# Optimization experiments

Hardware: AMD Instinct MI355X
Metric: run time of the kernel (lower is better)

The kernel has to match this reference:

```python
import jax, jax.numpy as jnp
import numpy as np

TEMP = 0.07  # temperature used as logits / 0.07 in the original


def setup_inputs() -> dict:
    key = jax.random.key(0)
    k1, k2, k3 = jax.random.split(key, 3)
    B, N, T, L, D = 8, 128, 8, 6, 256
    meta = jax.random.normal(k1, (B, N, T, L, D), dtype=jnp.float32)
    thing = jax.random.randint(k2, (B, N, T), 0, 2, dtype=jnp.int32)
    label = jax.random.randint(k3, (B, N, T), 0, 40, dtype=jnp.int32)
    return {"meta_weight_for_con": meta, "thing_gt_idx": thing, "label_tmp": label}


def _con_loss(meta, thing, label):
    # meta: [B,N,T,L,D]; thing,label: [B,N,T]
    B, N, T, L, D = meta.shape
    P = N * T
    valid = thing.reshape(B, P).astype(bool)            # [B,P] boolean gt mask
    lab = label.reshape(B, P)                           # [B,P]
    # meta_weight_b[mask] -> [K,L,D]; permute(1,0,2) -> per-layer [K,D].
    # We keep all P positions and mask instead of compacting (jit-friendly).
    w = meta.reshape(B, P, L, D).transpose(0, 2, 1, 3)  # [B,L,P,D]
    w = w / jnp.maximum(jnp.linalg.norm(w, axis=-1, keepdims=True), 1e-12)  # F.normalize
    z = jnp.einsum('blpd,blqd->blpq', w, w) / TEMP      # similarity / temp [B,L,P,P]

    same = lab[:, :, None] == lab[:, None, :]           # [B,P,P]
    vpair = valid[:, :, None] & valid[:, None, :]
    eye = jnp.eye(P, dtype=bool)
    pos_mask = same & (~eye) & vpair                    # positives: same label, not self
    neg_mask = (~same) & vpair                          # negatives: different label

    K = valid.sum(axis=1)                               # [B] ins_num_ per batch
    pos_count = pos_mask.sum(axis=-1)                   # [B,P]
    neg_count = neg_mask.sum(axis=-1)                   # [B,P]

    # --- random positive sample per (batch, layer, row), mirroring np.random.choice ---
    u = jax.random.uniform(jax.random.key(42), (B, L, P))
    r = jnp.floor(u * pos_count[:, None, :].astype(u.dtype)).astype(jnp.int32)
    r = jnp.minimum(r, jnp.maximum(pos_count - 1, 0)[:, None, :])
    ranks = jnp.cumsum(pos_mask, axis=-1) - 1           # rank of each positive in index order
    sel = pos_mask[:, None, :, :] & (ranks[:, None, :, :] == r[..., None])  # [B,L,P,P]
    zp = jnp.sum(jnp.where(sel, z, 0.0), axis=-1)       # chosen positive logit [B,L,P]
    diag = jnp.diagonal(z, axis1=-2, axis2=-1)          # self-sim fallback when no positives
    zp = jnp.where((pos_count > 0)[:, None, :], zp, diag)

    # --- last negative (original pads by repeating the last negative to K-1) ---
    iota = jnp.arange(P)
    idx_last = jnp.max(jnp.where(neg_mask, iota[None, None, :], -1), axis=-1)  # [B,P]
    idx = jnp.broadcast_to(jnp.maximum(idx_last, 0)[:, None, :, None], (B, L, P, 1))
    zl = jnp.take_along_axis(z, idx, axis=-1)[..., 0]   # [B,L,P]

    # --- stable CE with label 0: loss = lse(logits) - zp ---
    max_n = jnp.max(jnp.where(neg_mask[:, None], z, -jnp.inf), axis=-1)  # [B,L,P]
    m = jnp.maximum(zp, max_n)
    m = jnp.where(jnp.isfinite(m), m, zp)
    sum_neg = jnp.sum(jnp.where(neg_mask[:, None], jnp.exp(z - m[..., None]), 0.0), axis=-1)
    pad = jnp.maximum((K[:, None] - 1 - neg_count), 0).astype(z.dtype)   # [B,P]
    pad_term = pad[:, None, :] * jnp.where((neg_count > 0)[:, None, :], jnp.exp(zl - m), 0.0)
    loss_row = m + jnp.log(jnp.exp(zp - m) + sum_neg + pad_term) - zp    # [B,L,P]

    row_w = valid.astype(z.dtype)
    mean_per = jnp.sum(loss_row * row_w[:, None, :], axis=-1) / jnp.maximum(K, 1)[:, None].astype(z.dtype)  # [B,L]

    gate = jnp.sum((thing.sum(axis=2) > 0), axis=1) >= 2  # skip batches with <2 gt rows
    return jnp.sum(jnp.where(gate[:, None], mean_per, 0.0))


def reference(meta_weight_for_con, thing_gt_idx, label_tmp):
    return _con_loss(meta_weight_for_con, thing_gt_idx, label_tmp)
```

## Files before the change

kernel.cpp:

```cpp
#include <hip/hip_runtime.h>
#include <stdint.h>

namespace {

constexpr int Bb = 8, Ll = 6, Dd = 256, Pp = 1024;
constexpr float SCALE_Y = 14.285714285714286f * 1.4426950408889634f;
constexpr float M0y = 21.0f;
constexpr float LN2f = 0.6931471805599453f;

typedef __attribute__((ext_vector_type(4))) float floatx4;

__device__ const int PAIRS[36] = {
  0x00,0x01,0x02,0x03,0x04,0x05,0x06,0x07,
  0x11,0x12,0x13,0x14,0x15,0x16,0x17,
  0x22,0x23,0x24,0x25,0x26,0x27,
  0x33,0x34,0x35,0x36,0x37,
  0x44,0x45,0x46,0x47,
  0x55,0x56,0x57,
  0x66,0x67,
  0x77
};

__device__ __forceinline__ void async16(const void* g, void* l) {
  __builtin_amdgcn_global_load_lds(
      (const __attribute__((address_space(1))) void*)g,
      (__attribute__((address_space(3))) void*)l, 16, 0, 0);
}

__device__ __forceinline__ uint32_t rotl32(uint32_t x, int n) {
  return (x << n) | (x >> (32 - n));
}
__device__ __forceinline__ void tf_round(uint32_t& x0, uint32_t& x1, int r) {
  x0 += x1; x1 = rotl32(x1, r); x1 ^= x0;
}
__device__ void threefry2x32(uint32_t x0, uint32_t x1, uint32_t& o0, uint32_t& o1) {
  const uint32_t k0 = 0u, k1 = 42u;
  const uint32_t k2 = k0 ^ k1 ^ 0x1BD11BDAu;
  x0 += k0; x1 += k1;
  tf_round(x0,x1,13); tf_round(x0,x1,15); tf_round(x0,x1,26); tf_round(x0,x1,6);
  x0 += k1; x1 += k2 + 1u;
  tf_round(x0,x1,17); tf_round(x0,x1,29); tf_round(x0,x1,16); tf_round(x0,x1,24);
  x0 += k2; x1 += k0 + 2u;
  tf_round(x0,x1,13); tf_round(x0,x1,15); tf_round(x0,x1,26); tf_round(x0,x1,6);
  x0 += k0; x1 += k1 + 3u;
  tf_round(x0,x1,17); tf_round(x0,x1,29); tf_round(x0,x1,16); tf_round(x0,x1,24);
  x0 += k1; x1 += k2 + 4u;
  tf_round(x0,x1,13); tf_round(x0,x1,15); tf_round(x0,x1,26); tf_round(x0,x1,6);
  x0 += k2; x1 += k0 + 5u;
  o0 = x0; o1 = x1;
}
__device__ float jax_u01(uint32_t idx) {
  const uint32_t HALF = (uint32_t)(Bb * Ll * Pp / 2);
  uint32_t o0, o1, bits;
  if (idx < HALF) { threefry2x32(idx, idx + HALF, o0, o1); bits = o0; }
  else            { threefry2x32(idx - HALF, idx, o0, o1); bits = o1; }
  return __uint_as_float((bits >> 9) | 0x3f800000u) - 1.0f;
}

__device__ __forceinline__ uint32_t fp8e4m3_rne(float x) {
  uint32_t u = __float_as_uint(x);
  const uint32_t s = (u >> 24) & 0x80u;
  u &= 0x7FFFFFFFu;
  uint32_t code;
  if (u < 0x3C800000u) {
    code = (uint32_t)__float2int_rn(__uint_as_float(u) * 512.0f);
  } else {
    const uint32_t r = (u + 0x7FFFFu + ((u >> 20) & 1u)) >> 20;
    code = r - (120u << 3);
  }
  return s | code;
}
__device__ __forceinline__ float fp8e4m3_tof(uint32_t c) {
  const uint32_t e = (c >> 3) & 15u, m = c & 7u;
  float mag;
  if (e) mag = __uint_as_float(((e + 120u) << 23) | (m << 20));
  else   mag = (float)m * 0.001953125f;
  return (c & 0x80u) ? -mag : mag;
}

constexpr int NB_NORM = Bb * Pp * Ll / 4;
constexpr int NB_ROW  = Bb * Pp / 4;

__global__ void prep_k(const float* __restrict__ meta, const int* __restrict__ thing,
                       const int* __restrict__ label, uint8_t* __restrict__ wn,
                       int* __restrict__ qpos, int* __restrict__ negc,
                       int* __restrict__ qidx, int* __restrict__ Kv,
                       int* __restrict__ gatev, float* __restrict__ rowsum_g,
                       int* __restrict__ cnt, float* __restrict__ out) {
  __shared__ int sK[256], sG[256];
  const int bid = blockIdx.x, t = threadIdx.x;

  if (bid < NB_NORM) {
    const int wid = (bid * 256 + t) >> 6;
    const int lane = t & 63;
    const float4 v = *(const float4*)(meta + (size_t)wid * Dd + lane * 4);
    float ss = v.x * v.x + v.y * v.y + v.z * v.z + v.w * v.w;
    #pragma unroll
    for (int m = 32; m; m >>= 1) ss += __shfl_xor(ss, m, 64);
    const float inv = 1.0f / fmaxf(sqrtf(ss), 1e-12f);
    const int bp = wid / Ll, l = wid - bp * Ll;
    const int b = bp >> 10, p = bp & (Pp - 1);
    uint8_t* dst = wn + ((size_t)(b * Ll + l) * Pp + p) * Dd + lane * 4;
    const uint32_t packed = fp8e4m3_rne(v.x * inv)
                          | (fp8e4m3_rne(v.y * inv) << 8)
                          | (fp8e4m3_rne(v.z * inv) << 16)
                          | (fp8e4m3_rne(v.w * inv) << 24);
    *(uint32_t*)dst = packed;
    return;
  }
  if (bid < NB_NORM + NB_ROW) {
    const int wid = (bid - NB_NORM) * 4 + (t >> 6);
    const int lane = t & 63;
    const int b = wid >> 10, p = wid & (Pp - 1);
    const int* lab = label + b * Pp;
    const int* th  = thing + b * Pp;
    const int myLab = lab[p];
    const bool myValid = (th[p] != 0);

    uint32_t posbits = 0;
    int cntc[16];
    int pc = 0, nc = 0, last = -1;
    #pragma unroll
    for (int c = 0; c < 16; ++c) {
      const int q = c * 64 + lane;
      const int lq = lab[q];
      const bool vq = (th[q] != 0);
      const bool same = (lq == myLab);
      const bool pos = myValid && vq && same && (q != p);
      const bool neg = myValid && vq && !same;
      uint64_t bp2 = __ballot(pos);
      uint64_t bn = __ballot(neg);
      if (pos) posbits |= (1u << c);
      cntc[c] = __popcll(bp2);
      pc += cntc[c];
      nc += __popcll(bn);
      if (bn) last = c * 64 + 63 - __clzll(bn);
    }
    int qsel[Ll];
    #pragma unroll
    for (int l = 0; l < Ll; ++l) qsel[l] = p;
    if (pc > 0) {
      for (int l = 0; l < Ll; ++l) {
        const float u = jax_u01((uint32_t)((b * Ll + l) * Pp + p));
        int r = (int)floorf(u * (float)pc);
        r = min(r, pc - 1);
        int base = 0;
        for (int c = 0; c < 16; ++c) {
          if (r < base + cntc[c]) {
            const bool mine = (posbits >> c) & 1u;
            uint64_t bm = __ballot(mine);
            uint64_t ltmask = (lane == 0) ? 0ull : (~0ull >> (64 - lane));
            int myrank = __popcll(bm & ltmask);
            bool hit = mine && (base + myrank == r);
            uint64_t hb = __ballot(hit);
            qsel[l] = c * 64 + (int)__builtin_ctzll(hb);
            break;
          }
          base += cntc[c];
        }
      }
    }
    if (lane == 0) {
      negc[wid] = nc;
      qidx[wid] = (last < 0) ? 0 : last;
      #pragma unroll
      for (int l = 0; l < Ll; ++l) qpos[(b * Ll + l) * Pp + p] = qsel[l];
    }
    return;
  }
  if (bid < NB_NORM + NB_ROW + Bb) {
    const int b = bid - (NB_NORM + NB_ROW);
    int k = 0;
    for (int p = t; p < Pp; p += 256) k += (thing[b * Pp + p] != 0);
    int g = 0;
    if (t < 128) {
      int any = 0;
      for (int tt = 0; tt < 8; ++tt) any |= (thing[(b * 128 + t) * 8 + tt] != 0);
      g = any;
    }
    sK[t] = k; sG[t] = g;
    __syncthreads();
    for (int s = 128; s; s >>= 1) {
      if (t < s) { sK[t] += sK[t + s]; sG[t] += sG[t + s]; }
      __syncthreads();
    }
    if (t == 0) { Kv[b] = sK[0]; gatev[b] = (sG[0] >= 2) ? 1 : 0; }
    return;
  }
  if (bid < NB_NORM + NB_ROW + Bb + 48) {
    const int idx = (bid - (NB_NORM + NB_ROW + Bb)) * 256 + t;
    *(float4*)(rowsum_g + idx * 4) = (float4){0.f, 0.f, 0.f, 0.f};
    return;
  }
  if (t == 0) out[0] = 0.f;
  if (t < 48) cnt[t] = 0;
}

__global__ void zpzl_k(const uint8_t* __restrict__ wn,
                       const int* __restrict__ qpos, const int* __restrict__ qidx,
                       float* __restrict__ zp_g, float* __restrict__ zl_g) {
  const int wid = blockIdx.x * 4 + (threadIdx.x >> 6);
  const int lane = threadIdx.x & 63;
  const int bl = wid >> 10, p = wid & (Pp - 1);
  const int b = bl / Ll;
  const int qp = qpos[bl * Pp + p];
  const int qi = qidx[b * Pp + p];
  const uint8_t* W = wn + (size_t)bl * Pp * Dd;
  const uint32_t a4 = *(const uint32_t*)(W + (size_t)p  * Dd + lane * 4);
  const uint32_t b4 = *(const uint32_t*)(W + (size_t)qp * Dd + lane * 4);
  const uint32_t c4 = *(const uint32_t*)(W + (size_t)qi * Dd + lane * 4);
  float sp = 0.f, sl = 0.f;
  #pragma unroll
  for (int i = 0; i < 4; ++i) {
    const float a = fp8e4m3_tof((a4 >> (8 * i)) & 0xFF);
    sp += a * fp8e4m3_tof((b4 >> (8 * i)) & 0xFF);
    sl += a * fp8e4m3_tof((c4 >> (8 * i)) & 0xFF);
  }
  #pragma unroll
  for (int m = 32; m; m >>= 1) {
    sp += __shfl_xor(sp, m, 64);
    sl += __shfl_xor(sl, m, 64);
  }
  if (lane == 0) {
    zp_g[bl * Pp + p] = sp * SCALE_Y;
    zl_g[bl * Pp + p] = sl * SCALE_Y;
  }
}

__global__ __launch_bounds__(256)
void gemm_loss_k(const uint8_t* __restrict__ wn,
                 const int* __restrict__ thing, const int* __restrict__ label,
                 float* __restrict__ rowsum_g, const float* __restrict__ zp_g,
                 const float* __restrict__ zl_g, const int* __restrict__ negc,
                 const int* __restrict__ Kv, const int* __restrict__ gatev,
                 int* __restrict__ cnt, float* __restrict__ out) {
  __shared__ __align__(16) uint8_t As[128 * 256];
  __shared__ __align__(16) uint8_t Bs[128 * 256];
  __shared__ int labp_s[128], valp_s[128], labq_s[128], valq_s[128];
  __shared__ float rowsum_lds[128], colsum_lds[128];
  __shared__ int last_s;

  const int t = threadIdx.x;
  const int bid = blockIdx.x;
  const int xcd = bid & 7;
  const int chunk = bid >> 3;
  const int bl = xcd + 8 * (chunk % 6);
  const int b = bl / Ll;
  const int pair = PAIRS[chunk / 6];
  const int pt = pair >> 4, qt = pair & 15;
  const bool diag = (pt == qt);
  const int p0 = pt * 128, q0 = qt * 128;

  if (t < 128) {
    labp_s[t] = label[b * Pp + p0 + t];
    valp_s[t] = thing[b * Pp + p0 + t];
    labq_s[t] = label[b * Pp + q0 + t];
    valq_s[t] = thing[b * Pp + q0 + t];
    rowsum_lds[t] = 0.f;
    colsum_lds[t] = 0.f;
  }

  const uint8_t* Wbl = wn + (size_t)bl * Pp * Dd;
  const int lane = t & 63;
  const int w = t >> 6, wr = w >> 1, wc = w & 1;
  const int cq = lane & 15, rq = lane >> 4;
  const int wbase16 = (t & ~63) * 16;

  #pragma unroll
  for (int it = 0; it < 8; ++it) {
    const int c = it * 256 + t;
    const int row = c >> 4, sp = c & 15;
    const int sl = sp ^ (row & 15);
    async16(Wbl + (size_t)(p0 + row) * Dd + sl * 16, As + it * 4096 + wbase16);
    if (!diag)
      async16(Wbl + (size_t)(q0 + row) * Dd + sl * 16, Bs + it * 4096 + wbase16);
  }
  __syncthreads();

  const uint8_t* Bbase = diag ? As : Bs;

  floatx4 acc[4][4];
  #pragma unroll
  for (int i = 0; i < 4; ++i)
    #pragma unroll
    for (int j = 0; j < 4; ++j) acc[i][j] = (floatx4){0.f, 0.f, 0.f, 0.f};

  #pragma unroll
  for (int sub = 0; sub < 8; ++sub) {
    const int Lw = sub * 2 + (rq >> 1);
    const int off8 = (rq & 1) * 8;
    long long af[4], bf[4];
    #pragma unroll
    for (int fi = 0; fi < 4; ++fi) {
      const int row = wr * 64 + fi * 16 + cq;
      af[fi] = *(const long long*)(As + row * 256 + ((Lw ^ (row & 15)) << 4) + off8);
    }
    #pragma unroll
    for (int fj = 0; fj < 4; ++fj) {
      const int row = wc * 64 + fj * 16 + cq;
      bf[fj] = *(const long long*)(Bbase + row * 256 + ((Lw ^ (row & 15)) << 4) + off8);
    }
    #pragma unroll
    for (int fi = 0; fi < 4; ++fi)
      #pragma unroll
      for (int fj = 0; fj < 4; ++fj)
        acc[fi][fj] = __builtin_amdgcn_mfma_f32_16x16x32_fp8_fp8(af[fi], bf[fj],
                                                                 acc[fi][fj], 0, 0, 0);
  }

  int qlabv[4];
  float qvalf[4];
  float csum[4] = {0.f, 0.f, 0.f, 0.f};
  #pragma unroll
  for (int fj = 0; fj < 4; ++fj) {
    const int cl = wc * 64 + fj * 16 + cq;
    qlabv[fj] = labq_s[cl];
    qvalf[fj] = valq_s[cl] ? 1.f : 0.f;
  }
  #pragma unroll
  for (int fi = 0; fi < 4; ++fi) {
    #pragma unroll
    for (int reg = 0; reg < 4; ++reg) {
      const int rl = wr * 64 + fi * 16 + rq * 4 + reg;
      const int rlab = labp_s[rl];
      const float rvalf = valp_s[rl] ? 1.f : 0.f;
      float rsum = 0.f;
      #pragma unroll
      for (int fj = 0; fj < 4; ++fj) {
        const float y = acc[fi][fj][reg] * SCALE_Y;
        const float negm = (qlabv[fj] != rlab) ? (qvalf[fj] * rvalf) : 0.f;
        const float term = negm * exp2f(y - M0y);
        rsum += term;
        csum[fj] += term;
      }
      rsum += __shfl_xor(rsum, 1); rsum += __shfl_xor(rsum, 2);
      rsum += __shfl_xor(rsum, 4); rsum += __shfl_xor(rsum, 8);
      if (cq == 0) atomicAdd(&rowsum_lds[rl], rsum);
    }
  }
  if (!diag) {
    #pragma unroll
    for (int fj = 0; fj < 4; ++fj) {
      float c = csum[fj];
      c += __shfl_xor(c, 16); c += __shfl_xor(c, 32);
      if (rq == 0) atomicAdd(&colsum_lds[wc * 64 + fj * 16 + cq], c);
    }
  }
  __syncthreads();
  if (t < 128) {
    atomicAdd(&rowsum_g[bl * Pp + p0 + t], rowsum_lds[t]);
    if (!diag) atomicAdd(&rowsum_g[bl * Pp + q0 + t], colsum_lds[t]);
  }
  __syncthreads();
  if (t == 0) {
    __threadfence();
    last_s = (atomicAdd(&cnt[bl], 1) == 35);
  }
  __syncthreads();

  if (last_s) {
    __threadfence();
    const int Kb = Kv[b];
    const float invK = 1.f / (float)max(Kb, 1);
    float acc2 = 0.f;
    for (int p = t; p < Pp; p += 256) {
      if (thing[b * Pp + p] != 0) {
        const float yp = zp_g[bl * Pp + p], yl = zl_g[bl * Pp + p];
        const float rs = rowsum_g[bl * Pp + p];
        const int nc = negc[b * Pp + p];
        const float pad = fmaxf((float)(Kb - 1 - nc), 0.f);
        const float tot = exp2f(yp - M0y) + rs + ((nc > 0) ? pad * exp2f(yl - M0y) : 0.f);
        acc2 += LN2f * (M0y + log2f(tot) - yp) * invK;
      }
    }
    #pragma unroll
    for (int m = 32; m; m >>= 1) acc2 += __shfl_xor(acc2, m, 64);
    if (lane == 0) colsum_lds[w] = acc2;
    __syncthreads();
    if (t == 0 && gatev[b])
      atomicAdd(out, colsum_lds[0] + colsum_lds[1] + colsum_lds[2] + colsum_lds[3]);
  }
}

}

extern "C" void kernel_launch(void* const* d_in, const int* in_sizes, int n_in,
                              void* d_out, int out_size, void* d_ws, size_t ws_size,
                              hipStream_t stream) {
  const float* meta = (const float*)d_in[0];
  const int* thing  = (const int*)d_in[1];
  const int* label  = (const int*)d_in[2];
  float* out = (float*)d_out;

  char* ws = (char*)d_ws;
  size_t off = 0;
  uint8_t* wn = (uint8_t*)(ws + off); off += (size_t)Bb * Ll * Pp * Dd;
  int* qpos  = (int*)(ws + off); off += (size_t)Bb * Ll * Pp * 4;
  int* negc  = (int*)(ws + off); off += (size_t)Bb * Pp * 4;
  int* qidx  = (int*)(ws + off); off += (size_t)Bb * Pp * 4;
  int* Kv    = (int*)(ws + off); off += 64;
  int* gatev = (int*)(ws + off); off += 64;
  int* cnt   = (int*)(ws + off); off += 64 * 4;
  float* rowsum_g = (float*)(ws + off); off += (size_t)Bb * Ll * Pp * 4;
  float* zp_g     = (float*)(ws + off); off += (size_t)Bb * Ll * Pp * 4;
  float* zl_g     = (float*)(ws + off); off += (size_t)Bb * Ll * Pp * 4;

  const int nb_prep = NB_NORM + NB_ROW + Bb + 48 + 1;
  prep_k<<<nb_prep, 256, 0, stream>>>(meta, thing, label, wn, qpos, negc, qidx,
                                      Kv, gatev, rowsum_g, cnt, out);
  zpzl_k<<<(Bb * Ll * Pp) / 4, 256, 0, stream>>>(wn, qpos, qidx, zp_g, zl_g);
  gemm_loss_k<<<1728, 256, 0, stream>>>(wn, thing, label, rowsum_g, zp_g, zl_g,
                                        negc, Kv, gatev, cnt, out);
}
```

Measured before the change: 175.5 us.

## Fuse positive/last-logit dot products into GEMM diag tiles and split K staging

Removes the separate zpzl kernel and computes the chosen-positive and last-index logits inside the diagonal tiles of the GEMM loss kernel, writing them before the completion counter so the last block can consume them. The K dimension is also staged in two 128-byte chunks, halving LDS per block to allow more resident blocks. This trades an extra barrier pair per K step and extra work on diagonal blocks for one fewer launch and higher occupancy.

```diff
diff --git a/kernel.cpp b/kernel.cpp
--- a/kernel.cpp
+++ b/kernel.cpp
@@ -196,46 +196,16 @@
   if (t < 48) cnt[t] = 0;
 }
 
-__global__ void zpzl_k(const uint8_t* __restrict__ wn,
-                       const int* __restrict__ qpos, const int* __restrict__ qidx,
-                       float* __restrict__ zp_g, float* __restrict__ zl_g) {
-  const int wid = blockIdx.x * 4 + (threadIdx.x >> 6);
-  const int lane = threadIdx.x & 63;
-  const int bl = wid >> 10, p = wid & (Pp - 1);
-  const int b = bl / Ll;
-  const int qp = qpos[bl * Pp + p];
-  const int qi = qidx[b * Pp + p];
-  const uint8_t* W = wn + (size_t)bl * Pp * Dd;
-  const uint32_t a4 = *(const uint32_t*)(W + (size_t)p  * Dd + lane * 4);
-  const uint32_t b4 = *(const uint32_t*)(W + (size_t)qp * Dd + lane * 4);
-  const uint32_t c4 = *(const uint32_t*)(W + (size_t)qi * Dd + lane * 4);
-  float sp = 0.f, sl = 0.f;
-  #pragma unroll
-  for (int i = 0; i < 4; ++i) {
-    const float a = fp8e4m3_tof((a4 >> (8 * i)) & 0xFF);
-    sp += a * fp8e4m3_tof((b4 >> (8 * i)) & 0xFF);
-    sl += a * fp8e4m3_tof((c4 >> (8 * i)) & 0xFF);
-  }
-  #pragma unroll
-  for (int m = 32; m; m >>= 1) {
-    sp += __shfl_xor(sp, m, 64);
-    sl += __shfl_xor(sl, m, 64);
-  }
-  if (lane == 0) {
-    zp_g[bl * Pp + p] = sp * SCALE_Y;
-    zl_g[bl * Pp + p] = sl * SCALE_Y;
-  }
-}
-
 __global__ __launch_bounds__(256)
 void gemm_loss_k(const uint8_t* __restrict__ wn,
                  const int* __restrict__ thing, const int* __restrict__ label,
-                 float* __restrict__ rowsum_g, const float* __restrict__ zp_g,
-                 const float* __restrict__ zl_g, const int* __restrict__ negc,
+                 const int* __restrict__ qpos, const int* __restrict__ qidx,
+                 float* __restrict__ rowsum_g, float* __restrict__ zp_g,
+                 float* __restrict__ zl_g, const int* __restrict__ negc,
                  const int* __restrict__ Kv, const int* __restrict__ gatev,
                  int* __restrict__ cnt, float* __restrict__ out) {
-  __shared__ __align__(16) uint8_t As[128 * 256];
-  __shared__ __align__(16) uint8_t Bs[128 * 256];
+  __shared__ __align__(16) uint8_t As[128 * 128];
+  __shared__ __align__(16) uint8_t Bs[128 * 128];
   __shared__ int labp_s[128], valp_s[128], labq_s[128], valq_s[128];
   __shared__ float rowsum_lds[128], colsum_lds[128];
   __shared__ int last_s;
@@ -266,46 +236,48 @@
   const int cq = lane & 15, rq = lane >> 4;
   const int wbase16 = (t & ~63) * 16;
 
-  #pragma unroll
-  for (int it = 0; it < 8; ++it) {
-    const int c = it * 256 + t;
-    const int row = c >> 4, sp = c & 15;
-    const int sl = sp ^ (row & 15);
-    async16(Wbl + (size_t)(p0 + row) * Dd + sl * 16, As + it * 4096 + wbase16);
-    if (!diag)
-      async16(Wbl + (size_t)(q0 + row) * Dd + sl * 16, Bs + it * 4096 + wbase16);
-  }
-  __syncthreads();
-
-  const uint8_t* Bbase = diag ? As : Bs;
-
   floatx4 acc[4][4];
   #pragma unroll
   for (int i = 0; i < 4; ++i)
     #pragma unroll
     for (int j = 0; j < 4; ++j) acc[i][j] = (floatx4){0.f, 0.f, 0.f, 0.f};
 
-  #pragma unroll
-  for (int sub = 0; sub < 8; ++sub) {
-    const int Lw = sub * 2 + (rq >> 1);
-    const int off8 = (rq & 1) * 8;
-    long long af[4], bf[4];
-    #pragma unroll
-    for (int fi = 0; fi < 4; ++fi) {
-      const int row = wr * 64 + fi * 16 + cq;
-      af[fi] = *(const long long*)(As + row * 256 + ((Lw ^ (row & 15)) << 4) + off8);
-    }
-    #pragma unroll
-    for (int fj = 0; fj < 4; ++fj) {
-      const int row = wc * 64 + fj * 16 + cq;
-      bf[fj] = *(const long long*)(Bbase + row * 256 + ((Lw ^ (row & 15)) << 4) + off8);
-    }
-    #pragma unroll
-    for (int fi = 0; fi < 4; ++fi)
-      #pragma unroll
-      for (int fj = 0; fj < 4; ++fj)
-        acc[fi][fj] = __builtin_amdgcn_mfma_f32_16x16x32_fp8_fp8(af[fi], bf[fj],
-                                                                 acc[fi][fj], 0, 0, 0);
+  const uint8_t* Bbase = diag ? As : Bs;
+
+  for (int k0 = 0; k0 < Dd; k0 += 128) {
+    __syncthreads();
+    #pragma unroll
+    for (int it = 0; it < 4; ++it) {
+      const int c = it * 256 + t;
+      const int row = c >> 3, sp = c & 7;
+      const int sl = sp ^ (row & 7);
+      async16(Wbl + (size_t)(p0 + row) * Dd + k0 + sl * 16, As + it * 4096 + wbase16);
+      if (!diag)
+        async16(Wbl + (size_t)(q0 + row) * Dd + k0 + sl * 16, Bs + it * 4096 + wbase16);
+    }
+    __syncthreads();
+    #pragma unroll
+    for (int sub = 0; sub < 4; ++sub) {
+      const int Lw = sub * 2 + (rq >> 1);
+      const int off8 = (rq & 1) * 8;
+      long long af[4], bf[4];
+      #pragma unroll
+      for (int fi = 0; fi < 4; ++fi) {
+        const int row = wr * 64 + fi * 16 + cq;
+        af[fi] = *(const long long*)(As + row * 128 + (Lw ^ (row & 7)) * 16 + off8);
+      }
+      #pragma unroll
+      for (int fj = 0; fj < 4; ++fj) {
+        const int row = wc * 64 + fj * 16 + cq;
+        bf[fj] = *(const long long*)(Bbase + row * 128 + (Lw ^ (row & 7)) * 16 + off8);
+      }
+      #pragma unroll
+      for (int fi = 0; fi < 4; ++fi)
+        #pragma unroll
+        for (int fj = 0; fj < 4; ++fj)
+          acc[fi][fj] = __builtin_amdgcn_mfma_f32_16x16x32_fp8_fp8(af[fi], bf[fj],
+                                                                   acc[fi][fj], 0, 0, 0);
+    }
   }
 
   int qlabv[4];
@@ -346,6 +318,34 @@
       if (rq == 0) atomicAdd(&colsum_lds[wc * 64 + fj * 16 + cq], c);
     }
   }
+
+  if (diag) {
+    for (int rr = 0; rr < 32; ++rr) {
+      const int p = p0 + w * 32 + rr;
+      const int qp = qpos[bl * Pp + p];
+      const int qi = qidx[b * Pp + p];
+      const uint32_t a4 = *(const uint32_t*)(Wbl + (size_t)p  * Dd + lane * 4);
+      const uint32_t b4 = *(const uint32_t*)(Wbl + (size_t)qp * Dd + lane * 4);
+      const uint32_t c4 = *(const uint32_t*)(Wbl + (size_t)qi * Dd + lane * 4);
+      float sp = 0.f, sl = 0.f;
+      #pragma unroll
+      for (int i = 0; i < 4; ++i) {
+        const float a = fp8e4m3_tof((a4 >> (8 * i)) & 0xFF);
+        sp += a * fp8e4m3_tof((b4 >> (8 * i)) & 0xFF);
+        sl += a * fp8e4m3_tof((c4 >> (8 * i)) & 0xFF);
+      }
+      #pragma unroll
+      for (int m = 32; m; m >>= 1) {
+        sp += __shfl_xor(sp, m, 64);
+        sl += __shfl_xor(sl, m, 64);
+      }
+      if (lane == 0) {
+        zp_g[bl * Pp + p] = sp * SCALE_Y;
+        zl_g[bl * Pp + p] = sl * SCALE_Y;
+      }
+    }
+  }
+
   __syncthreads();
   if (t < 128) {
     atomicAdd(&rowsum_g[bl * Pp + p0 + t], rowsum_lds[t]);
@@ -408,7 +408,6 @@
   const int nb_prep = NB_NORM + NB_ROW + Bb + 48 + 1;
   prep_k<<<nb_prep, 256, 0, stream>>>(meta, thing, label, wn, qpos, negc, qidx,
                                       Kv, gatev, rowsum_g, cnt, out);
-  zpzl_k<<<(Bb * Ll * Pp) / 4, 256, 0, stream>>>(wn, qpos, qidx, zp_g, zl_g);
-  gemm_loss_k<<<1728, 256, 0, stream>>>(wn, thing, label, rowsum_g, zp_g, zl_g,
-                                        negc, Kv, gatev, cnt, out);
-}
+  gemm_loss_k<<<1728, 256, 0, stream>>>(wn, thing, label, qpos, qidx, rowsum_g,
+                                        zp_g, zl_g, negc, Kv, gatev, cnt, out);
+}
```

After: 208.1 us. +18.6%, slower.
